# Optimization experiments

Hardware: AMD Instinct MI355X
Metric: run time of the kernel (lower is better)

Reference implementation:

```python
import jax, jax.numpy as jnp
import numpy as np

N_NODES = 100000
N_EDGES = 600000
HIDDEN = 128
LN_EPS = 1e-8


def setup_inputs() -> dict:
    key = jax.random.key(0)
    k1, k2, k3 = jax.random.split(key, 3)
    x = jax.random.normal(k1, (N_NODES, HIDDEN), dtype=jnp.float32)
    edge_index = jax.random.randint(k2, (2, N_EDGES), 0, N_NODES, dtype=jnp.int32)
    # GCNConv linear weight (glorot-ish scale) and bias
    W = jax.random.normal(k3, (HIDDEN, HIDDEN), dtype=jnp.float32) / np.sqrt(HIDDEN)
    b = jnp.zeros((HIDDEN,), dtype=jnp.float32)
    ln_gamma = jnp.ones((HIDDEN,), dtype=jnp.float32)
    ln_beta = jnp.zeros((HIDDEN,), dtype=jnp.float32)
    return {"x": x, "edge_index": edge_index, "W": W, "b": b,
            "ln_gamma": ln_gamma, "ln_beta": ln_beta}


def _gcn_layer(x, edge_index, W, b, ln_gamma, ln_beta):
    n = x.shape[0]
    # --- GCNConv (PyG semantics): add self-loops, sym-normalize, x@W, scatter ---
    loop = jnp.arange(n, dtype=edge_index.dtype)
    src = jnp.concatenate([edge_index[0], loop])  # [E+N]
    dst = jnp.concatenate([edge_index[1], loop])
    deg = jax.ops.segment_sum(jnp.ones_like(dst, dtype=x.dtype), dst,
                              num_segments=n)  # in-degree incl. self-loop
    dinv = jnp.where(deg > 0, jax.lax.rsqrt(deg), 0.0)
    norm = dinv[src] * dinv[dst]  # [E+N]
    h = x @ W  # [N, H]
    msg = h[src] * norm[:, None]  # gather + scale, [E+N, H]
    agg = jax.ops.segment_sum(msg, dst, num_segments=n) + b  # scatter-sum
    # --- ReLU -> (dropout = identity in eval) -> residual -> LayerNorm ---
    y = jax.nn.relu(agg) + x
    mu = jnp.mean(y, axis=-1, keepdims=True)
    var = jnp.mean(jnp.square(y - mu), axis=-1, keepdims=True)
    return (y - mu) * jax.lax.rsqrt(var + LN_EPS) * ln_gamma + ln_beta


def reference(x, edge_index, W, b, ln_gamma, ln_beta):
    return _gcn_layer(x, edge_index, W, b, ln_gamma, ln_beta)
```

## Files before the change

### kernel.cpp

```cpp
#include <hip/hip_runtime.h>

#define HID 128
#define CAP 32
#define BM 64
#define EUN 8

typedef unsigned short u16;
typedef unsigned int u32;
typedef __attribute__((ext_vector_type(8))) short short8v;
typedef __attribute__((ext_vector_type(4))) float f32x4;
typedef __attribute__((ext_vector_type(4))) u32 u32x4;

__device__ inline u16 f2bf(float f) {
    union { float f; u32 u; } c; c.f = f;
    u32 u = c.u;
    return (u16)((u + 0x7FFFu + ((u >> 16) & 1u)) >> 16);
}
__device__ inline u32 pack2(float lo, float hi) {
    return (u32)f2bf(lo) | ((u32)f2bf(hi) << 16);
}
__device__ inline float bflo(u32 u) {
    union { u32 u; float f; } c; c.u = u << 16; return c.f;
}
__device__ inline float bfhi(u32 u) {
    union { u32 u; float f; } c; c.u = u & 0xFFFF0000u; return c.f;
}
__device__ inline float bf2f(u16 b) {
    union { u32 u; float f; } c; c.u = ((u32)b) << 16; return c.f;
}

__global__ __launch_bounds__(256) void k_prep(const float* __restrict__ x,
                                              u16* __restrict__ xbf,
                                              const float* __restrict__ W,
                                              u16* __restrict__ wswz, int n) {
    int t = blockIdx.x * blockDim.x + threadIdx.x;
    if (t < n * 16) {
        int g = t >> 4, l = t & 15;
        const float4* p = (const float4*)&x[(size_t)g * HID + l * 8];
        float4 v0 = p[0], v1 = p[1];
        uint4 o;
        o.x = pack2(v0.x, v0.y);
        o.y = pack2(v0.z, v0.w);
        o.z = pack2(v1.x, v1.y);
        o.w = pack2(v1.z, v1.w);
        *(uint4*)&xbf[(size_t)g * HID + l * 8] = o;
    }
    if (t < 128 * 128) {
        int i = t & 7;
        int lane = (t >> 3) & 63;
        int ct = (t >> 9) & 7;
        int ks = t >> 12;
        int k = ks * 32 + (lane >> 4) * 8 + i;
        int col = ct * 16 + (lane & 15);
        wswz[t] = f2bf(W[k * HID + col]);
    }
}

__global__ __launch_bounds__(256) void k_countfill(const int* __restrict__ src,
                                                   const int* __restrict__ dst,
                                                   int* __restrict__ cnt,
                                                   int* __restrict__ csr, int e) {
    const int base = blockIdx.x * (256 * EUN) + threadIdx.x;
    int d[EUN], s[EUN], slot[EUN];
    #pragma unroll
    for (int u = 0; u < EUN; ++u) {
        int i = base + u * 256;
        if (i < e) {
            d[u] = __builtin_nontemporal_load(&dst[i]);
            s[u] = __builtin_nontemporal_load(&src[i]);
        }
    }
    #pragma unroll
    for (int u = 0; u < EUN; ++u)
        if (base + u * 256 < e) slot[u] = atomicAdd(&cnt[d[u]], 1);
    #pragma unroll
    for (int u = 0; u < EUN; ++u)
        if (base + u * 256 < e && slot[u] < CAP)
            csr[(size_t)d[u] * CAP + slot[u]] = s[u];
}

__global__ __launch_bounds__(256) void k_fused(const u16* __restrict__ xbf,
                                               const int* __restrict__ cnt,
                                               const int* __restrict__ csr,
                                               const u16* __restrict__ wswz,
                                               const float* __restrict__ bvec,
                                               const float* __restrict__ gamma,
                                               const float* __restrict__ beta,
                                               float* __restrict__ out, int n) {
    __shared__ uint4 lds4[1024];
    char* lds = (char*)lds4;
    const int tid = threadIdx.x;
    const int row0 = blockIdx.x * BM;

    {
        const int grp = tid >> 4;
        const int l16 = tid & 15;
        const int j8 = l16 * 8;
        #pragma unroll
        for (int k = 0; k < 4; ++k) {
            int r = grp * 4 + k;
            int g = row0 + r;
            uint4 pk = make_uint4(0, 0, 0, 0);
            if (g < n) {
                const int len = min(cnt[g], CAP);
                const float dd = rsqrtf((float)(cnt[g] + 1));
                float acc[8];
                {
                    float s2 = dd * dd;
                    u32x4 hv = *(const u32x4*)&xbf[(size_t)g * HID + j8];
                    acc[0] = bflo(hv.x) * s2; acc[1] = bfhi(hv.x) * s2;
                    acc[2] = bflo(hv.y) * s2; acc[3] = bfhi(hv.y) * s2;
                    acc[4] = bflo(hv.z) * s2; acc[5] = bfhi(hv.z) * s2;
                    acc[6] = bflo(hv.w) * s2; acc[7] = bfhi(hv.w) * s2;
                }
                const size_t off = (size_t)g * CAP;
                for (int base = 0; base < len; base += 16) {
                    int idx = base + l16;
                    int sk = csr[off + (idx < len ? idx : 0)];
                    float dv = (idx < len) ? rsqrtf((float)(cnt[sk] + 1)) : 0.f;
                    int mm = (min(16, len - base) + 3) & ~3;
                    for (int j = 0; j < mm; j += 4) {
                        int s0 = __shfl(sk, j + 0, 16);
                        int s1 = __shfl(sk, j + 1, 16);
                        int s2 = __shfl(sk, j + 2, 16);
                        int s3 = __shfl(sk, j + 3, 16);
                        float w0 = __shfl(dv, j + 0, 16) * dd;
                        float w1 = __shfl(dv, j + 1, 16) * dd;
                        float w2 = __shfl(dv, j + 2, 16) * dd;
                        float w3 = __shfl(dv, j + 3, 16) * dd;
                        u32x4 h0 = *(const u32x4*)&xbf[(size_t)s0 * HID + j8];
                        u32x4 h1 = *(const u32x4*)&xbf[(size_t)s1 * HID + j8];
                        u32x4 h2 = *(const u32x4*)&xbf[(size_t)s2 * HID + j8];
                        u32x4 h3 = *(const u32x4*)&xbf[(size_t)s3 * HID + j8];
                        acc[0] = fmaf(bflo(h0.x), w0, acc[0]); acc[1] = fmaf(bfhi(h0.x), w0, acc[1]);
                        acc[2] = fmaf(bflo(h0.y), w0, acc[2]); acc[3] = fmaf(bfhi(h0.y), w0, acc[3]);
                        acc[4] = fmaf(bflo(h0.z), w0, acc[4]); acc[5] = fmaf(bfhi(h0.z), w0, acc[5]);
                        acc[6] = fmaf(bflo(h0.w), w0, acc[6]); acc[7] = fmaf(bfhi(h0.w), w0, acc[7]);
                        acc[0] = fmaf(bflo(h1.x), w1, acc[0]); acc[1] = fmaf(bfhi(h1.x), w1, acc[1]);
                        acc[2] = fmaf(bflo(h1.y), w1, acc[2]); acc[3] = fmaf(bfhi(h1.y), w1, acc[3]);
                        acc[4] = fmaf(bflo(h1.z), w1, acc[4]); acc[5] = fmaf(bfhi(h1.z), w1, acc[5]);
                        acc[6] = fmaf(bflo(h1.w), w1, acc[6]); acc[7] = fmaf(bfhi(h1.w), w1, acc[7]);
                        acc[0] = fmaf(bflo(h2.x), w2, acc[0]); acc[1] = fmaf(bfhi(h2.x), w2, acc[1]);
                        acc[2] = fmaf(bflo(h2.y), w2, acc[2]); acc[3] = fmaf(bfhi(h2.y), w2, acc[3]);
                        acc[4] = fmaf(bflo(h2.z), w2, acc[4]); acc[5] = fmaf(bfhi(h2.z), w2, acc[5]);
                        acc[6] = fmaf(bflo(h2.w), w2, acc[6]); acc[7] = fmaf(bfhi(h2.w), w2, acc[7]);
                        acc[0] = fmaf(bflo(h3.x), w3, acc[0]); acc[1] = fmaf(bfhi(h3.x), w3, acc[1]);
                        acc[2] = fmaf(bflo(h3.y), w3, acc[2]); acc[3] = fmaf(bfhi(h3.y), w3, acc[3]);
                        acc[4] = fmaf(bflo(h3.z), w3, acc[4]); acc[5] = fmaf(bfhi(h3.z), w3, acc[5]);
                        acc[6] = fmaf(bflo(h3.w), w3, acc[6]); acc[7] = fmaf(bfhi(h3.w), w3, acc[7]);
                    }
                }
                pk.x = pack2(acc[0], acc[1]);
                pk.y = pack2(acc[2], acc[3]);
                pk.z = pack2(acc[4], acc[5]);
                pk.w = pack2(acc[6], acc[7]);
            }
            int byte = r * 256 + l16 * 16;
            byte ^= (r & 7) << 4;
            *(uint4*)(lds + byte) = pk;
        }
    }
    __syncthreads();

    const int w = tid >> 6;
    const int l = tid & 63;
    const int c15 = l & 15;
    const short8v* wfrag = (const short8v*)wswz;

    f32x4 acc[8];
    #pragma unroll
    for (int c = 0; c < 8; ++c) acc[c] = (f32x4){0.f, 0.f, 0.f, 0.f};

    #pragma unroll
    for (int ks = 0; ks < 4; ++ks) {
        int row = w * 16 + c15;
        int byte = row * 256 + ks * 64 + (l >> 4) * 16;
        byte ^= (row & 7) << 4;
        short8v a = *(const short8v*)(lds + byte);
        #pragma unroll
        for (int ct = 0; ct < 8; ++ct) {
            short8v b = wfrag[(ks * 8 + ct) * 64 + l];
            acc[ct] = __builtin_amdgcn_mfma_f32_16x16x32_bf16(a, b, acc[ct], 0, 0, 0);
        }
    }

    float bb[8], gg[8], bz[8];
    #pragma unroll
    for (int ct = 0; ct < 8; ++ct) {
        bb[ct] = bvec[ct * 16 + c15];
        gg[ct] = gamma[ct * 16 + c15];
        bz[ct] = beta[ct * 16 + c15];
    }
    #pragma unroll
    for (int j = 0; j < 4; ++j) {
        int gr = row0 + w * 16 + (l >> 4) * 4 + j;
        if (gr < n) {
            const u16* xr = xbf + (size_t)gr * HID + c15;
            float v[8];
            #pragma unroll
            for (int ct = 0; ct < 8; ++ct)
                v[ct] = fmaxf(acc[ct][j] + bb[ct], 0.f) + bf2f(xr[ct * 16]);
            float sum = 0.f;
            #pragma unroll
            for (int ct = 0; ct < 8; ++ct) sum += v[ct];
            #pragma unroll
            for (int o = 1; o < 16; o <<= 1) sum += __shfl_xor(sum, o, 16);
            float mu = sum * (1.0f / HID);
            float d[8], vs = 0.f;
            #pragma unroll
            for (int ct = 0; ct < 8; ++ct) { d[ct] = v[ct] - mu; vs = fmaf(d[ct], d[ct], vs); }
            #pragma unroll
            for (int o = 1; o < 16; o <<= 1) vs += __shfl_xor(vs, o, 16);
            float inv = rsqrtf(vs * (1.0f / HID) + 1e-8f);
            float* orow = out + (size_t)gr * HID + c15;
            #pragma unroll
            for (int ct = 0; ct < 8; ++ct)
                __builtin_nontemporal_store(fmaf(d[ct] * inv, gg[ct], bz[ct]), &orow[ct * 16]);
        }
    }
}

extern "C" void kernel_launch(void* const* d_in, const int* in_sizes, int n_in,
                              void* d_out, int out_size, void* d_ws, size_t ws_size,
                              hipStream_t stream) {
    const float* x     = (const float*)d_in[0];
    const int*   ei    = (const int*)d_in[1];
    const float* W     = (const float*)d_in[2];
    const float* b     = (const float*)d_in[3];
    const float* gamma = (const float*)d_in[4];
    const float* beta  = (const float*)d_in[5];
    float* out = (float*)d_out;

    const int n = in_sizes[0] / HID;
    const int e = in_sizes[1] / 2;
    const int* src = ei;
    const int* dst = ei + e;

    u16* xbf  = (u16*)d_ws;
    int* cnt  = (int*)(xbf + (size_t)n * HID);
    int* csr  = cnt + n;
    u16* wswz = (u16*)(csr + (size_t)n * CAP);

    hipMemsetAsync(cnt, 0, (size_t)n * sizeof(int), stream);
    k_prep<<<((size_t)n * 16 + 255) / 256, 256, 0, stream>>>(x, xbf, W, wswz, n);
    k_countfill<<<(e + 256 * EUN - 1) / (256 * EUN), 256, 0, stream>>>(src, dst, cnt, csr, e);
    k_fused<<<(n + BM - 1) / BM, 256, 0, stream>>>(
        xbf, cnt, csr, wswz, b, gamma, beta, out, n);
}
```

Baseline: 102.0 us.

## Gather neighbor features as FP8 and merge prep and CSR build kernels

The prep kernel now also writes an FP8 (e4m3) copy of x alongside the bf16 copy. The aggregation loop gathers neighbor rows from that FP8 copy and unpacks them with packed fp8-to-f32 conversions, halving gather bytes per edge. The separate x-conversion, weight-swizzle and count/fill kernels are merged into one launch with block-range dispatch, removing a launch and letting the phases overlap. The cost is a large loss of precision in the aggregated messages, which may break the accuracy tolerance.

```diff
diff --git a/kernel.cpp b/kernel.cpp
--- a/kernel.cpp
+++ b/kernel.cpp
@@ -8,6 +8,7 @@
 typedef unsigned short u16;
 typedef unsigned int u32;
 typedef __attribute__((ext_vector_type(8))) short short8v;
+typedef __attribute__((ext_vector_type(2))) float f32x2;
 typedef __attribute__((ext_vector_type(4))) float f32x4;
 typedef __attribute__((ext_vector_type(4))) u32 u32x4;
 
@@ -29,23 +30,37 @@
     union { u32 u; float f; } c; c.u = ((u32)b) << 16; return c.f;
 }
 
-__global__ __launch_bounds__(256) void k_prep(const float* __restrict__ x,
-                                              u16* __restrict__ xbf,
-                                              const float* __restrict__ W,
-                                              u16* __restrict__ wswz, int n) {
-    int t = blockIdx.x * blockDim.x + threadIdx.x;
-    if (t < n * 16) {
-        int g = t >> 4, l = t & 15;
-        const float4* p = (const float4*)&x[(size_t)g * HID + l * 8];
-        float4 v0 = p[0], v1 = p[1];
-        uint4 o;
-        o.x = pack2(v0.x, v0.y);
-        o.y = pack2(v0.z, v0.w);
-        o.z = pack2(v1.x, v1.y);
-        o.w = pack2(v1.z, v1.w);
-        *(uint4*)&xbf[(size_t)g * HID + l * 8] = o;
-    }
-    if (t < 128 * 128) {
+__global__ __launch_bounds__(256) void k_build(const float* __restrict__ x,
+                                               u16* __restrict__ xbf,
+                                               u32* __restrict__ x8,
+                                               const float* __restrict__ W,
+                                               u16* __restrict__ wswz,
+                                               const int* __restrict__ src,
+                                               const int* __restrict__ dst,
+                                               int* __restrict__ cnt,
+                                               int* __restrict__ csr,
+                                               int n, int e, int nbE) {
+    const int b = blockIdx.x;
+    if (b < nbE) {
+        const int base = b * (256 * EUN) + threadIdx.x;
+        int d[EUN], s[EUN], slot[EUN];
+        #pragma unroll
+        for (int u = 0; u < EUN; ++u) {
+            int i = base + u * 256;
+            if (i < e) {
+                d[u] = __builtin_nontemporal_load(&dst[i]);
+                s[u] = __builtin_nontemporal_load(&src[i]);
+            }
+        }
+        #pragma unroll
+        for (int u = 0; u < EUN; ++u)
+            if (base + u * 256 < e) slot[u] = atomicAdd(&cnt[d[u]], 1);
+        #pragma unroll
+        for (int u = 0; u < EUN; ++u)
+            if (base + u * 256 < e && slot[u] < CAP)
+                csr[(size_t)d[u] * CAP + slot[u]] = s[u];
+    } else if (b < nbE + 64) {
+        int t = (b - nbE) * 256 + threadIdx.x;
         int i = t & 7;
         int lane = (t >> 3) & 63;
         int ct = (t >> 9) & 7;
@@ -53,33 +68,31 @@
         int k = ks * 32 + (lane >> 4) * 8 + i;
         int col = ct * 16 + (lane & 15);
         wswz[t] = f2bf(W[k * HID + col]);
-    }
-}
-
-__global__ __launch_bounds__(256) void k_countfill(const int* __restrict__ src,
-                                                   const int* __restrict__ dst,
-                                                   int* __restrict__ cnt,
-                                                   int* __restrict__ csr, int e) {
-    const int base = blockIdx.x * (256 * EUN) + threadIdx.x;
-    int d[EUN], s[EUN], slot[EUN];
-    #pragma unroll
-    for (int u = 0; u < EUN; ++u) {
-        int i = base + u * 256;
-        if (i < e) {
-            d[u] = __builtin_nontemporal_load(&dst[i]);
-            s[u] = __builtin_nontemporal_load(&src[i]);
-        }
-    }
-    #pragma unroll
-    for (int u = 0; u < EUN; ++u)
-        if (base + u * 256 < e) slot[u] = atomicAdd(&cnt[d[u]], 1);
-    #pragma unroll
-    for (int u = 0; u < EUN; ++u)
-        if (base + u * 256 < e && slot[u] < CAP)
-            csr[(size_t)d[u] * CAP + slot[u]] = s[u];
+    } else {
+        int t = (b - nbE - 64) * 256 + threadIdx.x;
+        if (t < n * 16) {
+            int g = t >> 4, l = t & 15;
+            const f32x4* p = (const f32x4*)&x[(size_t)g * HID + l * 8];
+            f32x4 v0 = __builtin_nontemporal_load(p);
+            f32x4 v1 = __builtin_nontemporal_load(p + 1);
+            uint4 o;
+            o.x = pack2(v0.x, v0.y);
+            o.y = pack2(v0.z, v0.w);
+            o.z = pack2(v1.x, v1.y);
+            o.w = pack2(v1.z, v1.w);
+            *(uint4*)&xbf[(size_t)g * HID + l * 8] = o;
+            u32 a = (u32)__builtin_amdgcn_cvt_pk_fp8_f32(v0.x, v0.y, 0, false);
+            a = (u32)__builtin_amdgcn_cvt_pk_fp8_f32(v0.z, v0.w, a, true);
+            u32 bq = (u32)__builtin_amdgcn_cvt_pk_fp8_f32(v1.x, v1.y, 0, false);
+            bq = (u32)__builtin_amdgcn_cvt_pk_fp8_f32(v1.z, v1.w, bq, true);
+            uint2 o8 = make_uint2(a, bq);
+            *(uint2*)&x8[(size_t)g * 32 + l * 2] = o8;
+        }
+    }
 }
 
 __global__ __launch_bounds__(256) void k_fused(const u16* __restrict__ xbf,
+                                               const u32* __restrict__ x8,
                                                const int* __restrict__ cnt,
                                                const int* __restrict__ csr,
                                                const u16* __restrict__ wswz,
@@ -128,26 +141,43 @@
                         float w1 = __shfl(dv, j + 1, 16) * dd;
                         float w2 = __shfl(dv, j + 2, 16) * dd;
                         float w3 = __shfl(dv, j + 3, 16) * dd;
-                        u32x4 h0 = *(const u32x4*)&xbf[(size_t)s0 * HID + j8];
-                        u32x4 h1 = *(const u32x4*)&xbf[(size_t)s1 * HID + j8];
-                        u32x4 h2 = *(const u32x4*)&xbf[(size_t)s2 * HID + j8];
-                        u32x4 h3 = *(const u32x4*)&xbf[(size_t)s3 * HID + j8];
-                        acc[0] = fmaf(bflo(h0.x), w0, acc[0]); acc[1] = fmaf(bfhi(h0.x), w0, acc[1]);
-                        acc[2] = fmaf(bflo(h0.y), w0, acc[2]); acc[3] = fmaf(bfhi(h0.y), w0, acc[3]);
-                        acc[4] = fmaf(bflo(h0.z), w0, acc[4]); acc[5] = fmaf(bfhi(h0.z), w0, acc[5]);
-                        acc[6] = fmaf(bflo(h0.w), w0, acc[6]); acc[7] = fmaf(bfhi(h0.w), w0, acc[7]);
-                        acc[0] = fmaf(bflo(h1.x), w1, acc[0]); acc[1] = fmaf(bfhi(h1.x), w1, acc[1]);
-                        acc[2] = fmaf(bflo(h1.y), w1, acc[2]); acc[3] = fmaf(bfhi(h1.y), w1, acc[3]);
-                        acc[4] = fmaf(bflo(h1.z), w1, acc[4]); acc[5] = fmaf(bfhi(h1.z), w1, acc[5]);
-                        acc[6] = fmaf(bflo(h1.w), w1, acc[6]); acc[7] = fmaf(bfhi(h1.w), w1, acc[7]);
-                        acc[0] = fmaf(bflo(h2.x), w2, acc[0]); acc[1] = fmaf(bfhi(h2.x), w2, acc[1]);
-                        acc[2] = fmaf(bflo(h2.y), w2, acc[2]); acc[3] = fmaf(bfhi(h2.y), w2, acc[3]);
-                        acc[4] = fmaf(bflo(h2.z), w2, acc[4]); acc[5] = fmaf(bfhi(h2.z), w2, acc[5]);
-                        acc[6] = fmaf(bflo(h2.w), w2, acc[6]); acc[7] = fmaf(bfhi(h2.w), w2, acc[7]);
-                        acc[0] = fmaf(bflo(h3.x), w3, acc[0]); acc[1] = fmaf(bfhi(h3.x), w3, acc[1]);
-                        acc[2] = fmaf(bflo(h3.y), w3, acc[2]); acc[3] = fmaf(bfhi(h3.y), w3, acc[3]);
-                        acc[4] = fmaf(bflo(h3.z), w3, acc[4]); acc[5] = fmaf(bfhi(h3.z), w3, acc[5]);
-                        acc[6] = fmaf(bflo(h3.w), w3, acc[6]); acc[7] = fmaf(bfhi(h3.w), w3, acc[7]);
+                        uint2 h0 = *(const uint2*)&x8[(size_t)s0 * 32 + l16 * 2];
+                        uint2 h1 = *(const uint2*)&x8[(size_t)s1 * 32 + l16 * 2];
+                        uint2 h2 = *(const uint2*)&x8[(size_t)s2 * 32 + l16 * 2];
+                        uint2 h3 = *(const uint2*)&x8[(size_t)s3 * 32 + l16 * 2];
+                        f32x2 p0, p1, p2, p3;
+                        p0 = __builtin_amdgcn_cvt_pk_f32_fp8(h0.x, false);
+                        p1 = __builtin_amdgcn_cvt_pk_f32_fp8(h0.x, true);
+                        p2 = __builtin_amdgcn_cvt_pk_f32_fp8(h0.y, false);
+                        p3 = __builtin_amdgcn_cvt_pk_f32_fp8(h0.y, true);
+                        acc[0] = fmaf(p0.x, w0, acc[0]); acc[1] = fmaf(p0.y, w0, acc[1]);
+                        acc[2] = fmaf(p1.x, w0, acc[2]); acc[3] = fmaf(p1.y, w0, acc[3]);
+                        acc[4] = fmaf(p2.x, w0, acc[4]); acc[5] = fmaf(p2.y, w0, acc[5]);
+                        acc[6] = fmaf(p3.x, w0, acc[6]); acc[7] = fmaf(p3.y, w0, acc[7]);
+                        p0 = __builtin_amdgcn_cvt_pk_f32_fp8(h1.x, false);
+                        p1 = __builtin_amdgcn_cvt_pk_f32_fp8(h1.x, true);
+                        p2 = __builtin_amdgcn_cvt_pk_f32_fp8(h1.y, false);
+                        p3 = __builtin_amdgcn_cvt_pk_f32_fp8(h1.y, true);
+                        acc[0] = fmaf(p0.x, w1, acc[0]); acc[1] = fmaf(p0.y, w1, acc[1]);
+                        acc[2] = fmaf(p1.x, w1, acc[2]); acc[3] = fmaf(p1.y, w1, acc[3]);
+                        acc[4] = fmaf(p2.x, w1, acc[4]); acc[5] = fmaf(p2.y, w1, acc[5]);
+                        acc[6] = fmaf(p3.x, w1, acc[6]); acc[7] = fmaf(p3.y, w1, acc[7]);
+                        p0 = __builtin_amdgcn_cvt_pk_f32_fp8(h2.x, false);
+                        p1 = __builtin_amdgcn_cvt_pk_f32_fp8(h2.x, true);
+                        p2 = __builtin_amdgcn_cvt_pk_f32_fp8(h2.y, false);
+                        p3 = __builtin_amdgcn_cvt_pk_f32_fp8(h2.y, true);
+                        acc[0] = fmaf(p0.x, w2, acc[0]); acc[1] = fmaf(p0.y, w2, acc[1]);
+                        acc[2] = fmaf(p1.x, w2, acc[2]); acc[3] = fmaf(p1.y, w2, acc[3]);
+                        acc[4] = fmaf(p2.x, w2, acc[4]); acc[5] = fmaf(p2.y, w2, acc[5]);
+                        acc[6] = fmaf(p3.x, w2, acc[6]); acc[7] = fmaf(p3.y, w2, acc[7]);
+                        p0 = __builtin_amdgcn_cvt_pk_f32_fp8(h3.x, false);
+                        p1 = __builtin_amdgcn_cvt_pk_f32_fp8(h3.x, true);
+                        p2 = __builtin_amdgcn_cvt_pk_f32_fp8(h3.y, false);
+                        p3 = __builtin_amdgcn_cvt_pk_f32_fp8(h3.y, true);
+                        acc[0] = fmaf(p0.x, w3, acc[0]); acc[1] = fmaf(p0.y, w3, acc[1]);
+                        acc[2] = fmaf(p1.x, w3, acc[2]); acc[3] = fmaf(p1.y, w3, acc[3]);
+                        acc[4] = fmaf(p2.x, w3, acc[4]); acc[5] = fmaf(p2.y, w3, acc[5]);
+                        acc[6] = fmaf(p3.x, w3, acc[6]); acc[7] = fmaf(p3.y, w3, acc[7]);
                     }
                 }
                 pk.x = pack2(acc[0], acc[1]);
@@ -237,13 +267,17 @@
     const int* dst = ei + e;
 
     u16* xbf  = (u16*)d_ws;
-    int* cnt  = (int*)(xbf + (size_t)n * HID);
+    u32* x8   = (u32*)(xbf + (size_t)n * HID);
+    int* cnt  = (int*)(x8 + (size_t)n * 32);
     int* csr  = cnt + n;
     u16* wswz = (u16*)(csr + (size_t)n * CAP);
 
+    const int nbE = (e + 256 * EUN - 1) / (256 * EUN);
+    const int nbS = (n * 16 + 255) / 256;
+
     hipMemsetAsync(cnt, 0, (size_t)n * sizeof(int), stream);
-    k_prep<<<((size_t)n * 16 + 255) / 256, 256, 0, stream>>>(x, xbf, W, wswz, n);
-    k_countfill<<<(e + 256 * EUN - 1) / (256 * EUN), 256, 0, stream>>>(src, dst, cnt, csr, e);
+    k_build<<<nbE + 64 + nbS, 256, 0, stream>>>(
+        x, xbf, x8, W, wswz, src, dst, cnt, csr, n, e, nbE);
     k_fused<<<(n + BM - 1) / BM, 256, 0, stream>>>(
-        xbf, cnt, csr, wswz, b, gamma, beta, out, n);
-}
+        xbf, x8, cnt, csr, wswz, b, gamma, beta, out, n);
+}
```

Result: slower. 109.4 us (+7.3%).
